# Kernel tuning notes

Hardware: AMD Instinct MI355X
Metric: run time of the kernel (lower is better)

The kernel has to match this reference:

```python
import jax, jax.numpy as jnp
import numpy as np

B, C, H, W = 32, 128, 56, 56
KSEL = 2            # gate columns (experts selected per sample)
E = 8               # expert_per_task
KN = 128            # kernel_num
KS = 3              # kernel_size
PAD = (KS - 1) // 2


def setup_inputs() -> dict:
    key = jax.random.key(0)
    k1, k2, k3, k4 = jax.random.split(key, 4)
    x = jax.random.normal(k1, (B, C, H, W), dtype=jnp.float32)
    gate = jax.random.randint(k2, (B, KSEL), 0, E, dtype=jnp.int32)
    conv_special_param = jax.random.normal(k3, (E, KN, C, KS, KS), dtype=jnp.float32) * 0.05
    conv_channel_param = jax.random.normal(k4, (E, C, C + KN, 1, 1), dtype=jnp.float32) * 0.05
    return {"x": x, "gate": gate,
            "conv_special_param": conv_special_param,
            "conv_channel_param": conv_channel_param}


def _per_sample_conv(xb, wb):
    # xb: [C, H+2p, W+2p], wb: [KN, C, KS, KS] -> [KN, H, W]
    out = jax.lax.conv_general_dilated(
        xb[None], wb, window_strides=(1, 1), padding='VALID',
        dimension_numbers=('NCHW', 'OIHW', 'NCHW'))
    return out[0]


def reference(x, gate, conv_special_param, conv_channel_param):
    px = jnp.pad(x, ((0, 0), (0, 0), (PAD, PAD), (PAD, PAD)))

    def per_gate(idx):  # idx: [B] expert indices for this gate column
        w_spec = conv_special_param[idx]                 # [B, KN, C, KS, KS]
        nf = jax.vmap(_per_sample_conv)(px, w_spec)      # [B, KN, H, W]
        cated = jnp.concatenate([x, nf], axis=1)         # [B, C+KN, H, W]
        w_ch = conv_channel_param[idx][..., 0, 0]        # [B, C, C+KN]
        return jnp.einsum('boc,bchw->bohw', w_ch, cated)  # [B, C, H, W]

    # stack over gate columns -> [B, KSEL, C, H, W]
    return jax.vmap(per_gate, in_axes=1, out_axes=1)(gate)
```

## Files before the change

kernel.cpp:

```cpp
#include <hip/hip_runtime.h>
#include <hip/hip_bf16.h>

#define B_   32
#define C_   128
#define H_   56
#define W_   56
#define KSEL 2
#define E_   8
#define KN_  128

typedef __attribute__((ext_vector_type(8))) short short8;
typedef __attribute__((ext_vector_type(4))) float f32x4;

static __device__ __forceinline__ ushort f2bf(float f) {
  union { float f; uint u; } v; v.f = f;
  uint u = v.u;
  return (ushort)((u + 0x7fffu + ((u >> 16) & 1u)) >> 16);
}

__global__ __launch_bounds__(256) void prep_x_kernel(
    const float* __restrict__ x, ushort* __restrict__ xh) {
  const int hp = blockIdx.x;
  const int b  = blockIdx.y;
  const int tid = threadIdx.x;
  ushort* rowp = xh + (size_t)(b * 58 + hp) * 58 * 128;

  if (hp == 0 || hp == 57) {
    uint4 z = make_uint4(0, 0, 0, 0);
    for (int l = tid; l < 464; l += 256) ((uint4*)rowp)[l] = z;
    return;
  }
  const int h = hp - 1;
  __shared__ __align__(16) ushort sT[56 * 136];

  const float* xb = x + (size_t)b * C_ * H_ * W_ + h * W_;
#pragma unroll
  for (int it = 0; it < 7; ++it) {
    int i4 = tid + it * 256;
    int c  = i4 / 14;
    int w4 = (i4 - c * 14) * 4;
    float4 v = *(const float4*)(xb + (size_t)c * (H_ * W_) + w4);
    sT[(w4 + 0) * 136 + c] = f2bf(v.x);
    sT[(w4 + 1) * 136 + c] = f2bf(v.y);
    sT[(w4 + 2) * 136 + c] = f2bf(v.z);
    sT[(w4 + 3) * 136 + c] = f2bf(v.w);
  }
  __syncthreads();
  for (int l = tid; l < 896; l += 256) {
    int w = l >> 4, sub = l & 15;
    uint4 v = *(const uint4*)&sT[w * 136 + sub * 8];
    *(uint4*)(rowp + (size_t)(w + 1) * 128 + sub * 8) = v;
  }
  if (tid < 32) {
    int wp = (tid < 16) ? 0 : 57;
    uint4 z = make_uint4(0, 0, 0, 0);
    *(uint4*)(rowp + (size_t)wp * 128 + (tid & 15) * 8) = z;
  }
}

__global__ __launch_bounds__(256) void fuse_weights_kernel(
    const float* __restrict__ Ws,
    const float* __restrict__ Wch,
    ushort* __restrict__ Weff) {
  const int e  = blockIdx.x;
  const int o0 = blockIdx.y * 32;
  const int c0 = blockIdx.z * 32;
  const int tid = threadIdx.x;
  const int ol = tid >> 3;
  const int cq = (tid & 7) * 4;

  __shared__ __align__(16) float sA[32 * 129];
  __shared__ __align__(16) float sB[32 * 32 * 12];

#pragma unroll
  for (int it = 0; it < 4; ++it) {
    int i4 = tid + it * 256;
    int o  = i4 >> 5;
    int kk = (i4 & 31) * 4;
    float4 v = *(const float4*)(Wch + (size_t)(e * C_ + o0 + o) * 256 + 128 + kk);
    sA[o * 129 + kk + 0] = v.x;
    sA[o * 129 + kk + 1] = v.y;
    sA[o * 129 + kk + 2] = v.z;
    sA[o * 129 + kk + 3] = v.w;
  }

  float acc[9][4];
#pragma unroll
  for (int j = 0; j < 9; ++j)
#pragma unroll
    for (int c2 = 0; c2 < 4; ++c2) acc[j][c2] = 0.f;

  for (int k0 = 0; k0 < 128; k0 += 32) {
    __syncthreads();
    {
      int k = tid >> 3, seg = tid & 7;
      const float* src = Ws + ((size_t)(e * KN_ + k0 + k) * C_ + c0) * 9 + seg * 36;
      float vb[36];
#pragma unroll
      for (int q = 0; q < 9; ++q) {
        float4 v = *(const float4*)(src + q * 4);
        vb[q * 4 + 0] = v.x; vb[q * 4 + 1] = v.y;
        vb[q * 4 + 2] = v.z; vb[q * 4 + 3] = v.w;
      }
      int c = seg * 4, j = 0;
#pragma unroll
      for (int m = 0; m < 36; ++m) {
        sB[(k * 32 + c) * 12 + j] = vb[m];
        if (++j == 9) { j = 0; ++c; }
      }
    }
    __syncthreads();
    for (int k = 0; k < 32; ++k) {
      float a = sA[ol * 129 + k0 + k];
#pragma unroll
      for (int c2 = 0; c2 < 4; ++c2) {
        const float* bp = &sB[(k * 32 + cq + c2) * 12];
#pragma unroll
        for (int j = 0; j < 9; ++j) acc[j][c2] += a * bp[j];
      }
    }
  }

  const int o = o0 + ol;
#pragma unroll
  for (int c2 = 0; c2 < 4; ++c2)
    acc[4][c2] += Wch[(size_t)(e * C_ + o) * 256 + c0 + cq + c2];

  const int nt   = (o0 >> 4) + (ol >> 4);
  const int lane = ((cq >> 3) << 4) | (ol & 15);
#pragma unroll
  for (int j = 0; j < 9; ++j) {
    uint lo = (uint)f2bf(acc[j][0]) | ((uint)f2bf(acc[j][1]) << 16);
    uint hi = (uint)f2bf(acc[j][2]) | ((uint)f2bf(acc[j][3]) << 16);
    size_t base = ((((size_t)(e * 9 + j) * 8 + nt) * 4 + blockIdx.z) * 64 + lane) * 8
                  + (cq & 4);
    *(uint2*)(Weff + base) = make_uint2(lo, hi);
  }
}

#define XSTR 40
#define OSTR 228

__global__ __launch_bounds__(256, 3) void conv_mfma_kernel(
    const ushort* __restrict__ xh,
    const int* __restrict__ gate,
    const ushort* __restrict__ Weff,
    float* __restrict__ out) {
  const int P   = blockIdx.x;
  const int xcd = P & 7;
  const int s   = P >> 3;
  const int bl  = s / 28;
  const int r1  = s - bl * 28;
  const int g   = r1 / 14;
  const int ht  = r1 - g * 14;
  const int b   = xcd * 4 + bl;
  const int bg  = b * 2 + g;
  const int h0  = ht * 4;
  const int e   = gate[bg];

  const int tid = threadIdx.x;
  const int wv = tid >> 6, lane = tid & 63;
  const int l15 = lane & 15, kq = lane >> 4;
  const int mh = wv >> 1, nh = wv & 1;

  __shared__ __align__(16) char smem[32 * OSTR * 4];
  ushort* sX = (ushort*)smem;
  float*  sO = (float*)smem;

  f32x4 acc[7][4];
#pragma unroll
  for (int t = 0; t < 7; ++t)
#pragma unroll
    for (int i = 0; i < 4; ++i) acc[t][i] = (f32x4){0.f, 0.f, 0.f, 0.f};

  int addr0[7];
#pragma unroll
  for (int t = 0; t < 7; ++t) {
    int p = mh * 112 + t * 16 + l15;
    int r = p / 56;
    int w = p - r * 56;
    addr0[t] = (r * 58 + w) * XSTR + kq * 8;
  }

  const ushort* xb = xh + (size_t)b * 58 * 58 * 128;
  const ushort* wlane = Weff + (size_t)e * (9 * 8 * 4 * 64 * 8)
                             + (size_t)(nh * 4) * (4 * 64 * 8)
                             + (size_t)lane * 8;

  for (int cc = 0; cc < 4; ++cc) {
    const int c0 = cc * 32;
    __syncthreads();
    for (int l = tid; l < 1392; l += 256) {
      int row = l / 232;
      int rem = l - row * 232;
      int col = rem >> 2, sub = rem & 3;
      uint4 v = *(const uint4*)(xb + ((size_t)(h0 + row) * 58 + col) * 128 + c0 + sub * 8);
      *(uint4*)&sX[(row * 58 + col) * XSTR + sub * 8] = v;
    }
    __syncthreads();
#pragma unroll
    for (int dy = 0; dy < 3; ++dy) {
#pragma unroll
      for (int dx = 0; dx < 3; ++dx) {
        const int j = dy * 3 + dx;
        short8 bfr[4];
#pragma unroll
        for (int i = 0; i < 4; ++i)
          bfr[i] = *(const short8*)(wlane + (size_t)j * (8 * 4 * 64 * 8)
                                          + (size_t)i * (4 * 64 * 8)
                                          + (size_t)cc * (64 * 8));
        const int ao = (dy * 58 + dx) * XSTR;
#pragma unroll
        for (int t = 0; t < 7; ++t) {
          short8 a = *(const short8*)&sX[addr0[t] + ao];
#pragma unroll
          for (int i = 0; i < 4; ++i)
            acc[t][i] = __builtin_amdgcn_mfma_f32_16x16x32_bf16(a, bfr[i], acc[t][i], 0, 0, 0);
        }
      }
    }
  }

  __syncthreads();
  for (int gq = 0; gq < 4; ++gq) {
    if (nh == (gq >> 1)) {
      const int gg = gq & 1;
#pragma unroll
      for (int ii = 0; ii < 2; ++ii) {
        const int i = gg * 2 + ii;
#pragma unroll
        for (int t = 0; t < 7; ++t) {
          int p0 = mh * 112 + t * 16 + kq * 4;
          int r  = p0 / 56;
          int w0 = p0 - r * 56;
          *(float4*)&sO[(ii * 16 + l15) * OSTR + r * 56 + w0] =
              make_float4(acc[t][i][0], acc[t][i][1], acc[t][i][2], acc[t][i][3]);
        }
      }
    }
    __syncthreads();
    {
      float* ob = out + ((size_t)bg * C_ + 32 * gq) * (H_ * W_) + (size_t)h0 * W_;
#pragma unroll
      for (int k = 0; k < 7; ++k) {
        int idx = k * 256 + tid;
        int ol  = idx / 56;
        int pos = idx - ol * 56;
        float4 v = *(const float4*)&sO[ol * OSTR + pos * 4];
        *(float4*)(ob + (size_t)ol * (H_ * W_) + pos * 4) = v;
      }
    }
    __syncthreads();
  }
}

extern "C" void kernel_launch(void* const* d_in, const int* in_sizes, int n_in,
                              void* d_out, int out_size, void* d_ws, size_t ws_size,
                              hipStream_t stream) {
  const float* x    = (const float*)d_in[0];
  const int*   gate = (const int*)d_in[1];
  const float* Ws   = (const float*)d_in[2];
  const float* Wch  = (const float*)d_in[3];
  float* out = (float*)d_out;

  ushort* xh   = (ushort*)d_ws;
  ushort* Weff = xh + (size_t)32 * 58 * 58 * 128;

  dim3 g0(58, 32);
  prep_x_kernel<<<g0, 256, 0, stream>>>(x, xh);

  dim3 g1(8, 4, 4);
  fuse_weights_kernel<<<g1, 256, 0, stream>>>(Ws, Wch, Weff);

  dim3 g2(896);
  conv_mfma_kernel<<<g2, 256, 0, stream>>>(xh, gate, Weff, out);
}
```

Baseline: 241.2 us.

## Split padded bf16 input into channel-chunk planes and read A fragments from global

The padded bf16 copy of x is re-laid out as four 32-channel planes per sample, so each 3x3 tap reads a contiguous 16-byte cell. The conv kernel no longer stages input tiles in LDS with barriers around each chunk; A fragments are loaded straight from global/L2. This removes the LDS fill and its syncs, but adds repeated global loads per tap (nine taps times seven tiles) and relies on cache hits for reuse.

```diff
diff --git a/kernel.cpp b/kernel.cpp
--- a/kernel.cpp
+++ b/kernel.cpp
@@ -18,16 +18,23 @@
   return (ushort)((u + 0x7fffu + ((u >> 16) & 1u)) >> 16);
 }
 
+#define CELL_US 32
+#define ROW_US  1856
+#define PLANE_US (58 * ROW_US)
+
 __global__ __launch_bounds__(256) void prep_x_kernel(
     const float* __restrict__ x, ushort* __restrict__ xh) {
   const int hp = blockIdx.x;
   const int b  = blockIdx.y;
   const int tid = threadIdx.x;
-  ushort* rowp = xh + (size_t)(b * 58 + hp) * 58 * 128;
 
   if (hp == 0 || hp == 57) {
     uint4 z = make_uint4(0, 0, 0, 0);
-    for (int l = tid; l < 464; l += 256) ((uint4*)rowp)[l] = z;
+#pragma unroll
+    for (int cc = 0; cc < 4; ++cc) {
+      ushort* rp = xh + (size_t)(b * 4 + cc) * PLANE_US + (size_t)hp * ROW_US;
+      for (int l = tid; l < 232; l += 256) ((uint4*)rp)[l] = z;
+    }
     return;
   }
   const int h = hp - 1;
@@ -46,15 +53,14 @@
     sT[(w4 + 3) * 136 + c] = f2bf(v.w);
   }
   __syncthreads();
-  for (int l = tid; l < 896; l += 256) {
-    int w = l >> 4, sub = l & 15;
-    uint4 v = *(const uint4*)&sT[w * 136 + sub * 8];
-    *(uint4*)(rowp + (size_t)(w + 1) * 128 + sub * 8) = v;
-  }
-  if (tid < 32) {
-    int wp = (tid < 16) ? 0 : 57;
-    uint4 z = make_uint4(0, 0, 0, 0);
-    *(uint4*)(rowp + (size_t)wp * 128 + (tid & 15) * 8) = z;
+  for (int q = tid; q < 928; q += 256) {
+    int cc   = q / 232, rem = q - cc * 232;
+    int cell = rem >> 2, sub = rem & 3;
+    uint4 v = make_uint4(0, 0, 0, 0);
+    if (cell >= 1 && cell <= 56)
+      v = *(const uint4*)&sT[(cell - 1) * 136 + cc * 32 + sub * 8];
+    ushort* rp = xh + (size_t)(b * 4 + cc) * PLANE_US + (size_t)hp * ROW_US;
+    *(uint4*)(rp + cell * CELL_US + sub * 8) = v;
   }
 }
 
@@ -138,7 +144,6 @@
   }
 }
 
-#define XSTR 40
 #define OSTR 228
 
 __global__ __launch_bounds__(256, 3) void conv_mfma_kernel(
@@ -163,9 +168,7 @@
   const int l15 = lane & 15, kq = lane >> 4;
   const int mh = wv >> 1, nh = wv & 1;
 
-  __shared__ __align__(16) char smem[32 * OSTR * 4];
-  ushort* sX = (ushort*)smem;
-  float*  sO = (float*)smem;
+  __shared__ __align__(16) float sO[32 * OSTR];
 
   f32x4 acc[7][4];
 #pragma unroll
@@ -173,31 +176,23 @@
 #pragma unroll
     for (int i = 0; i < 4; ++i) acc[t][i] = (f32x4){0.f, 0.f, 0.f, 0.f};
 
-  int addr0[7];
+  int aoff[7];
 #pragma unroll
   for (int t = 0; t < 7; ++t) {
     int p = mh * 112 + t * 16 + l15;
     int r = p / 56;
     int w = p - r * 56;
-    addr0[t] = (r * 58 + w) * XSTR + kq * 8;
-  }
-
-  const ushort* xb = xh + (size_t)b * 58 * 58 * 128;
+    aoff[t] = (h0 + r) * ROW_US + w * CELL_US + kq * 8;
+  }
+
+  const ushort* xb = xh + (size_t)(b * 4) * PLANE_US;
   const ushort* wlane = Weff + (size_t)e * (9 * 8 * 4 * 64 * 8)
                              + (size_t)(nh * 4) * (4 * 64 * 8)
                              + (size_t)lane * 8;
 
   for (int cc = 0; cc < 4; ++cc) {
-    const int c0 = cc * 32;
-    __syncthreads();
-    for (int l = tid; l < 1392; l += 256) {
-      int row = l / 232;
-      int rem = l - row * 232;
-      int col = rem >> 2, sub = rem & 3;
-      uint4 v = *(const uint4*)(xb + ((size_t)(h0 + row) * 58 + col) * 128 + c0 + sub * 8);
-      *(uint4*)&sX[(row * 58 + col) * XSTR + sub * 8] = v;
-    }
-    __syncthreads();
+    const ushort* xcc = xb + (size_t)cc * PLANE_US;
+    const ushort* wcc = wlane + cc * (64 * 8);
 #pragma unroll
     for (int dy = 0; dy < 3; ++dy) {
 #pragma unroll
@@ -206,13 +201,12 @@
         short8 bfr[4];
 #pragma unroll
         for (int i = 0; i < 4; ++i)
-          bfr[i] = *(const short8*)(wlane + (size_t)j * (8 * 4 * 64 * 8)
-                                          + (size_t)i * (4 * 64 * 8)
-                                          + (size_t)cc * (64 * 8));
-        const int ao = (dy * 58 + dx) * XSTR;
+          bfr[i] = *(const short8*)(wcc + (size_t)j * (8 * 4 * 64 * 8)
+                                        + (size_t)i * (4 * 64 * 8));
+        const int ao = dy * ROW_US + dx * CELL_US;
 #pragma unroll
         for (int t = 0; t < 7; ++t) {
-          short8 a = *(const short8*)&sX[addr0[t] + ao];
+          short8 a = *(const short8*)(xcc + aoff[t] + ao);
 #pragma unroll
           for (int i = 0; i < 4; ++i)
             acc[t][i] = __builtin_amdgcn_mfma_f32_16x16x32_bf16(a, bfr[i], acc[t][i], 0, 0, 0);
@@ -221,7 +215,6 @@
     }
   }
 
-  __syncthreads();
   for (int gq = 0; gq < 4; ++gq) {
     if (nh == (gq >> 1)) {
       const int gg = gq & 1;
@@ -264,7 +257,7 @@
   float* out = (float*)d_out;
 
   ushort* xh   = (ushort*)d_ws;
-  ushort* Weff = xh + (size_t)32 * 58 * 58 * 128;
+  ushort* Weff = xh + (size_t)(32 * 4) * PLANE_US;
 
   dim3 g0(58, 32);
   prep_x_kernel<<<g0, 256, 0, stream>>>(x, xh);
```

Measured after the change: 359.5 us. 49.0% more time.
